# Kernel tuning notes

Measured on AMD Instinct MI355X. Metric: run time of the kernel, lower is better.

## Reference

```python
import jax, jax.numpy as jnp
import numpy as np

B, H, W, DIM, WS, SHIFT, HEADS = 32, 56, 56, 256, 7, 3, 8
N = WS * WS          # 49 tokens per window
C2 = 2 * DIM         # concatenated two-modal channel dim
NW = (H // WS) * (W // WS)


def _rel_index(ws):
    coords = np.stack(np.meshgrid(np.arange(ws), np.arange(ws), indexing='ij')).reshape(2, -1)
    rel = (coords[:, :, None] - coords[:, None, :]).transpose(1, 2, 0)
    rel[:, :, 0] += ws - 1
    rel[:, :, 1] += ws - 1
    rel[:, :, 0] *= 2 * ws - 1
    return rel.sum(-1)  # (N, N) int

REL_IDX = _rel_index(WS).reshape(-1)


def _attn_mask():
    # standard Swin shifted-window mask: 0 / -100 per window pair
    img = np.zeros((H, W))
    cnt = 0
    for hs in (slice(0, H - WS), slice(H - WS, H - SHIFT), slice(H - SHIFT, H)):
        for ws_ in (slice(0, W - WS), slice(W - WS, W - SHIFT), slice(W - SHIFT, W)):
            img[hs, ws_] = cnt
            cnt += 1
    mw = img.reshape(H // WS, WS, W // WS, WS).transpose(0, 2, 1, 3).reshape(-1, N)
    d = mw[:, None, :] - mw[:, :, None]
    return np.where(d != 0, -100.0, 0.0).astype(np.float32)  # (nW, N, N)

ATTN_MASK = _attn_mask()


def _win_part(x):  # (B,H,W,C) -> (nW*B, N, C)
    b, c = x.shape[0], x.shape[-1]
    x = x.reshape(b, H // WS, WS, W // WS, WS, c).transpose(0, 1, 3, 2, 4, 5)
    return x.reshape(-1, N, c)


def _win_rev(w, b):  # (nW*B, N, C) -> (B,H,W,C)
    c = w.shape[-1]
    x = w.reshape(b, H // WS, W // WS, WS, WS, c).transpose(0, 1, 3, 2, 4, 5)
    return x.reshape(b, H, W, c)


def _ln(t, g, bb):
    m = t.mean(-1, keepdims=True)
    v = t.var(-1, keepdims=True)
    return (t - m) / jnp.sqrt(v + 1e-5) * g + bb


def setup_inputs() -> dict:
    key = jax.random.key(0)
    ks = jax.random.split(key, 8)
    def nrm(k, shape, s=0.02):
        return jax.random.normal(k, shape, jnp.float32) * s
    return {
        'x': jax.random.normal(ks[0], (B, H * W, DIM), jnp.float32),
        'y': jax.random.normal(ks[1], (B, H * W, DIM), jnp.float32),
        'g1': jnp.ones((DIM,), jnp.float32), 'b1': jnp.zeros((DIM,), jnp.float32),
        'rpb': nrm(ks[2], ((2 * WS - 1) * (2 * WS - 1), HEADS)),
        'w_qkv': nrm(ks[3], (6 * DIM, 2 * DIM)), 'b_qkv': jnp.zeros((6 * DIM,), jnp.float32),
        'w_proj': nrm(ks[4], (DIM, 2 * DIM)), 'b_proj': jnp.zeros((DIM,), jnp.float32),
        'g2': jnp.ones((DIM,), jnp.float32), 'b2': jnp.zeros((DIM,), jnp.float32),
        'w_fc1': nrm(ks[5], (4 * DIM, DIM)), 'b_fc1': jnp.zeros((4 * DIM,), jnp.float32),
        'w_fc2': nrm(ks[6], (DIM, 4 * DIM)), 'b_fc2': jnp.zeros((DIM,), jnp.float32),
    }


def reference(x, y, g1, b1, rpb, w_qkv, b_qkv, w_proj, b_proj, g2, b2, w_fc1, b_fc1, w_fc2, b_fc2):
    scale = (DIM // HEADS) ** -0.5  # as in __init__: head_dim = dim // num_heads
    shortcut = x
    xn = _ln(x, g1, b1).reshape(B, H, W, DIM)
    yn = _ln(y, g1, b1).reshape(B, H, W, DIM)
    # cyclic shift
    xn = jnp.roll(xn, (-SHIFT, -SHIFT), axis=(1, 2))
    yn = jnp.roll(yn, (-SHIFT, -SHIFT), axis=(1, 2))
    xw, yw = _win_part(xn), _win_part(yn)            # (nW*B, N, C)
    xy = jnp.concatenate([xw, yw], axis=-1)          # (nW*B, N, 2C)
    nwb, hd = xy.shape[0], C2 // HEADS
    qkv = (xy @ w_qkv.T + b_qkv).reshape(nwb, N, 3, HEADS, hd).transpose(2, 0, 3, 1, 4)
    q, k, v = qkv[0] * scale, qkv[1], qkv[2]         # (nW*B, h, N, d)
    attn = jnp.einsum('whnd,whmd->whnm', q, k)
    bias = rpb[REL_IDX].reshape(N, N, HEADS).transpose(2, 0, 1)  # (h, N, N)
    attn = attn + bias[None]
    attn = attn.reshape(B, NW, HEADS, N, N) + jnp.asarray(ATTN_MASK)[None, :, None]
    attn = jax.nn.softmax(attn.reshape(nwb, HEADS, N, N), axis=-1)
    out = jnp.einsum('whnm,whmd->whnd', attn, v).transpose(0, 2, 1, 3).reshape(nwb, N, C2)
    out = out @ w_proj.T + b_proj                    # fuse 2C -> C
    out = _win_rev(out, B)
    out = jnp.roll(out, (SHIFT, SHIFT), axis=(1, 2)).reshape(B, H * W, DIM)
    x = shortcut + out
    h = _ln(x, g2, b2)
    h = jax.nn.gelu(h @ w_fc1.T + b_fc1, approximate=False)
    return x + h @ w_fc2.T + b_fc2
```

## Files before the change

### kernel.cpp

```cpp
#include <hip/hip_runtime.h>
#include <hip/hip_bf16.h>

#define DEVI __device__ __forceinline__

typedef __attribute__((ext_vector_type(8))) short short8;
typedef __attribute__((ext_vector_type(4))) float f32x4;
typedef unsigned int u32;
typedef unsigned short u16;

typedef __attribute__((address_space(1))) const u32 gu32_t;
typedef __attribute__((address_space(3))) u32 lu32_t;

DEVI u16 f2bf(float f) {
  u32 u = __builtin_bit_cast(u32, f);
  u32 r = (u + 0x7fffu + ((u >> 16) & 1u)) >> 16;
  return (u16)r;
}

DEVI f32x4 mfma16(short8 a, short8 b, f32x4 c) {
  return __builtin_amdgcn_mfma_f32_16x16x32_bf16(a, b, c, 0, 0, 0);
}

DEVI void gload16(const void* g, void* l) {
  __builtin_amdgcn_global_load_lds((gu32_t*)g, (lu32_t*)l, 16, 0, 0);
}

DEVI float gelu_t(float v) {
  const float u = v * (0.7978845608f + 0.0356774081f * v * v);
  const float t = 1.0f - 2.0f / (__expf(2.0f * u) + 1.0f);
  return 0.5f * v * (1.0f + t);
}

#define CHUNK_ROWS 25088
#define PLANE ((size_t)CHUNK_ROWS * 64)
#define KOFF  ((size_t)8 * PLANE)
#define VOFF  ((size_t)16 * PLANE)

__global__ __launch_bounds__(256) void convk(const float* __restrict__ s, u16* __restrict__ d, int n4) {
  int i = blockIdx.x * 256 + threadIdx.x;
  if (i < n4) {
    const float4 v = ((const float4*)s)[i];
    ushort4 o;
    o.x = f2bf(v.x); o.y = f2bf(v.y); o.z = f2bf(v.z); o.w = f2bf(v.w);
    ((ushort4*)d)[i] = o;
  }
}

__global__ __launch_bounds__(256) void btab_build(const float* __restrict__ rpb, float* __restrict__ btab) {
  const int cls = blockIdx.x >> 3, h = blockIdx.x & 7;
  float* dst = btab + (size_t)(cls * 8 + h) * 4096;
  for (int e = threadIdx.x; e < 4096; e += 256) {
    const int n = e >> 6, m = e & 63;
    float v;
    if (m >= 49) {
      v = -1e30f;
    } else if (n >= 49) {
      v = 0.f;
    } else {
      const int r1 = n / 7, c1 = n - r1 * 7;
      const int r2 = m / 7, c2 = m - r2 * 7;
      const int rel = (r1 - r2 + 6) * 13 + (c1 - c2 + 6);
      v = rpb[rel * 8 + h];
      const int reg1 = ((cls & 1) ? (r1 < 4 ? 1 : 2) : 0) * 3 + ((cls & 2) ? (c1 < 4 ? 1 : 2) : 0);
      const int reg2 = ((cls & 1) ? (r2 < 4 ? 1 : 2) : 0) * 3 + ((cls & 2) ? (c2 < 4 ? 1 : 2) : 0);
      if (reg1 != reg2) v -= 100.f;
    }
    dst[e] = v;
  }
}

__global__ __launch_bounds__(256) void ln_gather(
    const float* __restrict__ x, const float* __restrict__ y,
    const float* __restrict__ g1, const float* __restrict__ b1,
    u16* __restrict__ XY, int rowbase)
{
  const int wv = threadIdx.x >> 6, lane = threadIdx.x & 63;
  const int rl = blockIdx.x * 4 + wv;
  const int row = rowbase + rl;
  const int w = row / 49, n = row - w * 49;
  const int b = w >> 6, win = w & 63, wh = win >> 3, ww = win & 7;
  const int r = n / 7, c = n - r * 7;
  int oh = wh * 7 + r + 3; if (oh >= 56) oh -= 56;
  int ow = ww * 7 + c + 3; if (ow >= 56) ow -= 56;
  const size_t po = ((size_t)b * 3136 + oh * 56 + ow) * 256;
  const float4 g1v = ((const float4*)g1)[lane];
  const float4 b1v = ((const float4*)b1)[lane];
  u16* orow = XY + (size_t)rl * 512;
  #pragma unroll
  for (int mod = 0; mod < 2; ++mod) {
    const float* src = (mod ? y : x) + po;
    const float4 v = ((const float4*)src)[lane];
    float s = v.x + v.y + v.z + v.w;
    #pragma unroll
    for (int off = 1; off < 64; off <<= 1) s += __shfl_xor(s, off);
    const float mean = s * (1.0f / 256.0f);
    const float d0 = v.x - mean, d1 = v.y - mean, d2 = v.z - mean, d3 = v.w - mean;
    float sq = d0 * d0 + d1 * d1 + d2 * d2 + d3 * d3;
    #pragma unroll
    for (int off = 1; off < 64; off <<= 1) sq += __shfl_xor(sq, off);
    const float rstd = rsqrtf(sq * (1.0f / 256.0f) + 1e-5f);
    ushort4 o;
    o.x = f2bf(d0 * rstd * g1v.x + b1v.x);
    o.y = f2bf(d1 * rstd * g1v.y + b1v.y);
    o.z = f2bf(d2 * rstd * g1v.z + b1v.z);
    o.w = f2bf(d3 * rstd * g1v.w + b1v.w);
    *(ushort4*)(orow + mod * 256 + lane * 4) = o;
  }
}

__global__ __launch_bounds__(256) void qkv_gemm(
    const u16* __restrict__ A, const u16* __restrict__ Bw,
    const float* __restrict__ bias, u16* __restrict__ Qo)
{
  __shared__ __align__(16) u16 sA[128 * 64];
  __shared__ __align__(16) u16 sB[128 * 64];
  const int nx = gridDim.x;
  const int nwg = nx * gridDim.y;
  const int orig = blockIdx.y * nx + blockIdx.x;
  const int sw = (orig & 7) * (nwg >> 3) + (orig >> 3);
  const int m0  = (sw / nx) * 128;
  const int nn0 = (sw % nx) * 128;
  const int tid = threadIdx.x;
  const int lane = tid & 63;
  const int wv = tid >> 6;
  const int wm = wv >> 1, wn = wv & 1;
  const int rq = lane & 15, kg = lane >> 4;
  f32x4 acc[4][4];
  #pragma unroll
  for (int i = 0; i < 4; ++i)
    #pragma unroll
    for (int j = 0; j < 4; ++j) acc[i][j] = f32x4{0,0,0,0};

  for (int kt = 0; kt < 8; ++kt) {
    if (kt) __syncthreads();
    #pragma unroll
    for (int i = 0; i < 4; ++i) {
      const int c = i * 256 + tid;
      gload16(A + (size_t)(m0 + (c >> 3)) * 512 + kt * 64 + (c & 7) * 8, sA + c * 8);
    }
    #pragma unroll
    for (int i = 0; i < 4; ++i) {
      const int c = i * 256 + tid;
      gload16(Bw + (size_t)(nn0 + (c >> 3)) * 512 + kt * 64 + (c & 7) * 8, sB + c * 8);
    }
    __syncthreads();
    #pragma unroll
    for (int k0 = 0; k0 < 2; ++k0) {
      short8 af[4], bf8[4];
      #pragma unroll
      for (int mt = 0; mt < 4; ++mt)
        af[mt] = *(const short8*)(sA + (wm * 64 + mt * 16 + rq) * 64 + k0 * 32 + kg * 8);
      #pragma unroll
      for (int nt = 0; nt < 4; ++nt)
        bf8[nt] = *(const short8*)(sB + (wn * 64 + nt * 16 + rq) * 64 + k0 * 32 + kg * 8);
      #pragma unroll
      for (int mt = 0; mt < 4; ++mt)
        #pragma unroll
        for (int nt = 0; nt < 4; ++nt)
          acc[mt][nt] = mfma16(af[mt], bf8[nt], acc[mt][nt]);
    }
  }
  #pragma unroll
  for (int mt = 0; mt < 4; ++mt) {
    #pragma unroll
    for (int nt = 0; nt < 4; ++nt) {
      const int col = nn0 + wn * 64 + nt * 16 + rq;
      const int t = col >> 9, rem = col & 511;
      const int h = rem >> 6, d = rem & 63;
      const float bc = bias[col];
      const float sc = (t == 0) ? 0.17677669529663687f : 1.0f;
      u16* bp = Qo + (size_t)(t * 8 + h) * PLANE + d;
      #pragma unroll
      for (int r = 0; r < 4; ++r) {
        const int row = m0 + wm * 64 + mt * 16 + kg * 4 + r;
        bp[(size_t)row * 64] = f2bf((acc[mt][nt][r] + bc) * sc);
      }
    }
  }
}

__global__ __launch_bounds__(256, 3) void attn3(
    const u16* __restrict__ qkv, const float* __restrict__ btab,
    u16* __restrict__ concat, int wbase)
{
  __shared__ __align__(16) u16 sP[4][3136];
  __shared__ __align__(16) u16 sVT[4][4608];

  const int tid = threadIdx.x;
  const int wv = tid >> 6, lane = tid & 63;
  const int rq = lane & 15, kg = lane >> 4;
  const int gw = blockIdx.x * 4 + wv;
  const int wl = gw >> 3, h = gw & 7;
  const int w = wbase + wl;
  const int win = w & 63, wh = win >> 3, ww = win & 7;
  const int cls = ((wh == 7) ? 1 : 0) | ((ww == 7) ? 2 : 0);
  const float* Tb = btab + (size_t)(cls * 8 + h) * 4096;
  u16* sPw = sP[wv];
  u16* sVw = sVT[wv];

  const u16* qbase = qkv + (size_t)h * PLANE + (size_t)wl * 49 * 64;
  const u16* kbase = qkv + KOFF + (size_t)h * PLANE + (size_t)wl * 49 * 64;
  const u16* vbase = qkv + VOFF + (size_t)h * PLANE + (size_t)wl * 49 * 64;

  short8 vreg[4][2];
  #pragma unroll
  for (int t = 0; t < 4; ++t)
    #pragma unroll
    for (int h2 = 0; h2 < 2; ++h2)
      vreg[t][h2] = *(const short8*)(vbase + (size_t)(16 * t + rq) * 64 + kg * 8 + h2 * 32);

  short8 ak[4][2];
  #pragma unroll
  for (int j = 0; j < 4; ++j) {
    const int rr = (16 * j + rq) > 48 ? 48 : (16 * j + rq);
    ak[j][0] = *(const short8*)(kbase + rr * 64 + kg * 8);
    ak[j][1] = *(const short8*)(kbase + rr * 64 + 32 + kg * 8);
  }
  f32x4 sacc[4][4];
  #pragma unroll
  for (int i = 0; i < 4; ++i)
    #pragma unroll
    for (int j = 0; j < 4; ++j) sacc[i][j] = f32x4{0,0,0,0};
  #pragma unroll
  for (int i = 0; i < 4; ++i) {
    const int rr = (16 * i + rq) > 48 ? 48 : (16 * i + rq);
    const short8 a0 = *(const short8*)(qbase + rr * 64 + kg * 8);
    const short8 a1 = *(const short8*)(qbase + rr * 64 + 32 + kg * 8);
    #pragma unroll
    for (int j = 0; j < 4; ++j) {
      sacc[i][j] = mfma16(a0, ak[j][0], sacc[i][j]);
      sacc[i][j] = mfma16(a1, ak[j][1], sacc[i][j]);
    }
  }

  #pragma unroll
  for (int t = 0; t < 4; ++t) {
    const int row = 16 * t + rq;
    #pragma unroll
    for (int h2 = 0; h2 < 2; ++h2) {
      const int c0 = kg * 8 + h2 * 32;
      #pragma unroll
      for (int j = 0; j < 8; ++j)
        sVw[(c0 + j) * 72 + (row ^ (kg << 4))] = (u16)vreg[t][h2][j];
    }
  }

  #pragma unroll
  for (int i = 0; i < 4; ++i) {
    #pragma unroll
    for (int r = 0; r < 4; ++r) {
      const int n = 16 * i + kg * 4 + r;
      const float* Trow = Tb + n * 64 + rq;
      float pv[4];
      #pragma unroll
      for (int j = 0; j < 4; ++j)
        pv[j] = sacc[i][j][r] + Trow[16 * j];
      float mx = fmaxf(fmaxf(pv[0], pv[1]), fmaxf(pv[2], pv[3]));
      #pragma unroll
      for (int off = 1; off < 16; off <<= 1) mx = fmaxf(mx, __shfl_xor(mx, off));
      float sm = 0.f;
      #pragma unroll
      for (int j = 0; j < 4; ++j) { const float e = __expf(pv[j] - mx); pv[j] = e; sm += e; }
      #pragma unroll
      for (int off = 1; off < 16; off <<= 1) sm += __shfl_xor(sm, off);
      const float inv = 1.0f / sm;
      if (n < 49) {
        #pragma unroll
        for (int j = 0; j < 4; ++j) {
          const int col = 16 * j + rq;
          sPw[n * 64 + (((col >> 3) ^ (n & 7)) << 3) + (col & 7)] = f2bf(pv[j] * inv);
        }
      }
    }
  }

  f32x4 oacc[4][4];
  #pragma unroll
  for (int i = 0; i < 4; ++i)
    #pragma unroll
    for (int j = 0; j < 4; ++j) oacc[i][j] = f32x4{0,0,0,0};
  #pragma unroll
  for (int m0v = 0; m0v < 2; ++m0v) {
    short8 av[4];
    #pragma unroll
    for (int ct = 0; ct < 4; ++ct) {
      const int col = ct * 16 + rq;
      const int s = (col >> 3) & 3;
      short8 vvv = *(const short8*)(sVw + col * 72 + ((m0v * 32 + kg * 8) ^ (s << 4)));
      if (m0v == 1) {
        if (kg == 3) {
          #pragma unroll
          for (int e = 0; e < 8; ++e) vvv[e] = 0;
        } else if (kg == 2) {
          #pragma unroll
          for (int e = 1; e < 8; ++e) vvv[e] = 0;
        }
      }
      av[ct] = vvv;
    }
    #pragma unroll
    for (int i = 0; i < 4; ++i) {
      const int rr = (16 * i + rq) > 48 ? 48 : (16 * i + rq);
      const int ch = (m0v * 4 + kg) ^ (rr & 7);
      const short8 pa = *(const short8*)(sPw + rr * 64 + ch * 8);
      #pragma unroll
      for (int ct = 0; ct < 4; ++ct)
        oacc[i][ct] = mfma16(pa, av[ct], oacc[i][ct]);
    }
  }

  __builtin_amdgcn_s_waitcnt(0);
  #pragma unroll
  for (int i = 0; i < 4; ++i)
    #pragma unroll
    for (int ct = 0; ct < 4; ++ct)
      #pragma unroll
      for (int r = 0; r < 4; ++r) {
        const int n = 16 * i + kg * 4 + r;
        if (n < 49) {
          const int col = ct * 16 + rq;
          sPw[n * 64 + (((col >> 3) ^ (n & 7)) << 3) + (col & 7)] = f2bf(oacc[i][ct][r]);
        }
      }
  u16* crow = concat + (size_t)(wl * 49) * 512 + h * 64;
  #pragma unroll
  for (int it = 0; it < 7; ++it) {
    const int c = it * 64 + lane;
    if (c < 392) {
      const int m = c >> 3, s = c & 7;
      const short8 vvv = *(const short8*)(sPw + m * 64 + ((s ^ (m & 7)) << 3));
      *(short8*)(crow + (size_t)m * 512 + s * 8) = vvv;
    }
  }
}

__global__ __launch_bounds__(256, 2) void projln(
    const u16* __restrict__ A, const u16* __restrict__ Bw,
    const float* __restrict__ bias, const float* __restrict__ x,
    const float* __restrict__ g2, const float* __restrict__ b2,
    float* __restrict__ out, u16* __restrict__ xn2, int rowbase)
{
  __shared__ __align__(16) u16 sA[128 * 64];
  __shared__ __align__(16) u16 sB[256 * 64];
  const int m0 = blockIdx.x * 128;
  const int tid = threadIdx.x;
  const int lane = tid & 63;
  const int wv = tid >> 6;
  const int rq = lane & 15, kg = lane >> 4;
  f32x4 acc[2][16];
  #pragma unroll
  for (int i = 0; i < 2; ++i)
    #pragma unroll
    for (int j = 0; j < 16; ++j) acc[i][j] = f32x4{0,0,0,0};

  for (int kt = 0; kt < 8; ++kt) {
    if (kt) __syncthreads();
    #pragma unroll
    for (int i = 0; i < 4; ++i) {
      const int c = i * 256 + tid;
      gload16(A + (size_t)(m0 + (c >> 3)) * 512 + kt * 64 + (c & 7) * 8, sA + c * 8);
    }
    #pragma unroll
    for (int i = 0; i < 8; ++i) {
      const int c = i * 256 + tid;
      gload16(Bw + (size_t)(c >> 3) * 512 + kt * 64 + (c & 7) * 8, sB + c * 8);
    }
    __syncthreads();
    #pragma unroll
    for (int k0 = 0; k0 < 2; ++k0) {
      short8 af[2];
      #pragma unroll
      for (int mt = 0; mt < 2; ++mt)
        af[mt] = *(const short8*)(sA + (wv * 32 + mt * 16 + rq) * 64 + k0 * 32 + kg * 8);
      #pragma unroll
      for (int nt = 0; nt < 16; ++nt) {
        const short8 bf8 = *(const short8*)(sB + (nt * 16 + rq) * 64 + k0 * 32 + kg * 8);
        #pragma unroll
        for (int mt = 0; mt < 2; ++mt)
          acc[mt][nt] = mfma16(af[mt], bf8, acc[mt][nt]);
      }
    }
  }

  float br[16], g2r[16], b2r[16];
  #pragma unroll
  for (int nt = 0; nt < 16; ++nt) {
    const int col = nt * 16 + rq;
    br[nt] = bias[col]; g2r[nt] = g2[col]; b2r[nt] = b2[col];
  }
  #pragma unroll
  for (int mt = 0; mt < 2; ++mt) {
    #pragma unroll
    for (int r = 0; r < 4; ++r) {
      const int row = m0 + wv * 32 + mt * 16 + kg * 4 + r;
      const u32 g = (u32)(rowbase + row);
      const u32 w = g / 49u; const u32 n = g - w * 49u;
      const int b = w >> 6, win = w & 63, wh = win >> 3, ww = win & 7;
      const u32 rr = n / 7u; const u32 cc = n - rr * 7u;
      int oh = wh * 7 + (int)rr + 3; if (oh >= 56) oh -= 56;
      int ow = ww * 7 + (int)cc + 3; if (ow >= 56) ow -= 56;
      const size_t po = ((size_t)b * 3136 + oh * 56 + ow) * 256;
      float vals[16];
      float s = 0.f;
      #pragma unroll
      for (int nt = 0; nt < 16; ++nt) {
        const float v = acc[mt][nt][r] + br[nt] + x[po + nt * 16 + rq];
        vals[nt] = v; s += v;
      }
      #pragma unroll
      for (int off = 1; off < 16; off <<= 1) s += __shfl_xor(s, off);
      const float mean = s * (1.0f / 256.0f);
      float sq = 0.f;
      #pragma unroll
      for (int nt = 0; nt < 16; ++nt) { const float d_ = vals[nt] - mean; sq += d_ * d_; }
      #pragma unroll
      for (int off = 1; off < 16; off <<= 1) sq += __shfl_xor(sq, off);
      const float rstd = rsqrtf(sq * (1.0f / 256.0f) + 1e-5f);
      #pragma unroll
      for (int nt = 0; nt < 16; ++nt) {
        const int col = nt * 16 + rq;
        out[po + col] = vals[nt];
        xn2[po + col] = f2bf((vals[nt] - mean) * rstd * g2r[nt] + b2r[nt]);
      }
    }
  }
}

__global__ __launch_bounds__(256, 3) void fused_mlp(
    const u16* __restrict__ xn2, const u16* __restrict__ w1,
    const float* __restrict__ bf1, const u16* __restrict__ w2,
    const float* __restrict__ bf2v, float* __restrict__ out)
{
  __shared__ __align__(16) u16 sX[64 * 256];
  __shared__ __align__(16) u16 sH[64 * 128];

  const int m0 = blockIdx.x * 64;
  const int tid = threadIdx.x;
  const int wv = tid >> 6, lane = tid & 63;
  const int rq = lane & 15, kg = lane >> 4;

  #pragma unroll
  for (int i = 0; i < 8; ++i) {
    const int c = i * 256 + tid;
    const int row = c >> 5, ch = c & 31;
    const int sch = (ch & 24) | ((ch ^ row) & 7);
    gload16(xn2 + (size_t)(m0 + row) * 256 + sch * 8, sX + c * 8);
  }

  f32x4 acc2[4][4];
  #pragma unroll
  for (int i = 0; i < 4; ++i)
    #pragma unroll
    for (int j = 0; j < 4; ++j) acc2[i][j] = f32x4{0,0,0,0};

  __syncthreads();

  for (int t = 0; t < 8; ++t) {
    f32x4 a1[4][2];
    #pragma unroll
    for (int i = 0; i < 4; ++i)
      #pragma unroll
      for (int j = 0; j < 2; ++j) a1[i][j] = f32x4{0,0,0,0};
    #pragma unroll
    for (int ks = 0; ks < 8; ++ks) {
      short8 bfr[2];
      #pragma unroll
      for (int nt = 0; nt < 2; ++nt)
        bfr[nt] = *(const short8*)(w1 + (size_t)(t * 128 + wv * 32 + nt * 16 + rq) * 256 + ks * 32 + kg * 8);
      #pragma unroll
      for (int mt = 0; mt < 4; ++mt) {
        const int R = mt * 16 + rq;
        const int wk = ks * 4 + kg;
        const short8 af = *(const short8*)(sX + R * 256 + ((wk & 24) | ((wk ^ R) & 7)) * 8);
        #pragma unroll
        for (int nt = 0; nt < 2; ++nt)
          a1[mt][nt] = mfma16(af, bfr[nt], a1[mt][nt]);
      }
    }
    __syncthreads();
    #pragma unroll
    for (int nt = 0; nt < 2; ++nt) {
      const int col = wv * 32 + nt * 16 + rq;
      const float bb = bf1[t * 128 + col];
      const int ch = col >> 3;
      #pragma unroll
      for (int mt = 0; mt < 4; ++mt)
        #pragma unroll
        for (int r = 0; r < 4; ++r) {
          const int row = mt * 16 + kg * 4 + r;
          sH[row * 128 + ((ch & 8) | ((ch ^ row) & 7)) * 8 + (col & 7)] =
              f2bf(gelu_t(a1[mt][nt][r] + bb));
        }
    }
    __syncthreads();
    #pragma unroll
    for (int ks = 0; ks < 4; ++ks) {
      short8 bfr2[4];
      #pragma unroll
      for (int nt = 0; nt < 4; ++nt)
        bfr2[nt] = *(const short8*)(w2 + (size_t)(wv * 64 + nt * 16 + rq) * 1024 + t * 128 + ks * 32 + kg * 8);
      #pragma unroll
      for (int mt = 0; mt < 4; ++mt) {
        const int R = mt * 16 + rq;
        const int wk = ks * 4 + kg;
        const short8 af = *(const short8*)(sH + R * 128 + ((wk & 8) | ((wk ^ R) & 7)) * 8);
        #pragma unroll
        for (int nt = 0; nt < 4; ++nt)
          acc2[mt][nt] = mfma16(af, bfr2[nt], acc2[mt][nt]);
      }
    }
  }

  #pragma unroll
  for (int nt = 0; nt < 4; ++nt) {
    const int col = wv * 64 + nt * 16 + rq;
    const float bb = bf2v[col];
    #pragma unroll
    for (int mt = 0; mt < 4; ++mt)
      #pragma unroll
      for (int r = 0; r < 4; ++r) {
        float* p = out + (size_t)(m0 + mt * 16 + kg * 4 + r) * 256 + col;
        *p = acc2[mt][nt][r] + bb + *p;
      }
  }
}

extern "C" void kernel_launch(void* const* d_in, const int* in_sizes, int n_in,
                              void* d_out, int out_size, void* d_ws, size_t ws_size,
                              hipStream_t stream) {
  const float* x      = (const float*)d_in[0];
  const float* y      = (const float*)d_in[1];
  const float* g1     = (const float*)d_in[2];
  const float* b1     = (const float*)d_in[3];
  const float* rpb    = (const float*)d_in[4];
  const float* w_qkv  = (const float*)d_in[5];
  const float* b_qkv  = (const float*)d_in[6];
  const float* w_proj = (const float*)d_in[7];
  const float* b_proj = (const float*)d_in[8];
  const float* g2     = (const float*)d_in[9];
  const float* b2     = (const float*)d_in[10];
  const float* w_fc1  = (const float*)d_in[11];
  const float* b_fc1  = (const float*)d_in[12];
  const float* w_fc2  = (const float*)d_in[13];
  const float* b_fc2  = (const float*)d_in[14];
  float* out = (float*)d_out;

  u16* wsp = (u16*)d_ws;
  u16* wqkv_bf  = wsp;
  u16* wproj_bf = wsp + 786432;
  u16* wfc1_bf  = wsp + 917504;
  u16* wfc2_bf  = wsp + 1179648;
  float* btab   = (float*)(wsp + 1441792);
  u16* xn2      = wsp + 1703936;
  u16* XYc      = wsp + 27394048;
  u16* qkvc     = wsp + 40239104;

  convk<<<768, 256, 0, stream>>>(w_qkv,  wqkv_bf,  196608);
  convk<<<128, 256, 0, stream>>>(w_proj, wproj_bf, 32768);
  convk<<<256, 256, 0, stream>>>(w_fc1,  wfc1_bf,  65536);
  convk<<<256, 256, 0, stream>>>(w_fc2,  wfc2_bf,  65536);
  btab_build<<<32, 256, 0, stream>>>(rpb, btab);

  for (int c = 0; c < 4; ++c) {
    ln_gather<<<6272, 256, 0, stream>>>(x, y, g1, b1, XYc, c * CHUNK_ROWS);
    qkv_gemm<<<dim3(12, 196), 256, 0, stream>>>(XYc, wqkv_bf, b_qkv, qkvc);
    attn3<<<1024, 256, 0, stream>>>(qkvc, btab, XYc, c * 512);
    projln<<<196, 256, 0, stream>>>(XYc, wproj_bf, b_proj, x, g2, b2, out, xn2, c * CHUNK_ROWS);
  }

  fused_mlp<<<1568, 256, 0, stream>>>(xn2, wfc1_bf, b_fc1, wfc2_bf, b_fc2, out);
}
```

Measured before the change: 866.2 us.

## Stage QKV epilogue through LDS for coalesced stores; widen MLP hidden chunk

The QKV GEMM epilogue now writes bias-added, scaled bf16 results into a swizzled shared-memory tile that reuses the operand buffers. It then issues 16-byte vector stores per head plane, replacing the previous scattered 2-byte stores with a 128-byte row stride. Separately, the fused MLP processes the 1024-wide hidden dimension in 4 chunks of 256 instead of 8 of 128. This halves the barrier/GELU round trips but doubles sH and the accumulator registers, and lowers the occupancy hint from 3 to 2 blocks per CU.

Result: no change. 854.1 us (-1.4%).

```diff
diff --git a/kernel.cpp b/kernel.cpp
--- a/kernel.cpp
+++ b/kernel.cpp
@@ -112,8 +112,9 @@
     const u16* __restrict__ A, const u16* __restrict__ Bw,
     const float* __restrict__ bias, u16* __restrict__ Qo)
 {
-  __shared__ __align__(16) u16 sA[128 * 64];
-  __shared__ __align__(16) u16 sB[128 * 64];
+  __shared__ __align__(16) u16 smem[128 * 128];
+  u16* sA = smem;
+  u16* sB = smem + 128 * 64;
   const int nx = gridDim.x;
   const int nwg = nx * gridDim.y;
   const int orig = blockIdx.y * nx + blockIdx.x;
@@ -160,22 +161,33 @@
           acc[mt][nt] = mfma16(af[mt], bf8[nt], acc[mt][nt]);
     }
   }
-  #pragma unroll
-  for (int mt = 0; mt < 4; ++mt) {
-    #pragma unroll
-    for (int nt = 0; nt < 4; ++nt) {
-      const int col = nn0 + wn * 64 + nt * 16 + rq;
-      const int t = col >> 9, rem = col & 511;
-      const int h = rem >> 6, d = rem & 63;
-      const float bc = bias[col];
-      const float sc = (t == 0) ? 0.17677669529663687f : 1.0f;
-      u16* bp = Qo + (size_t)(t * 8 + h) * PLANE + d;
+  __syncthreads();
+  const int t = nn0 >> 9;
+  const int hbase = (nn0 & 511) >> 6;
+  const float sc = (t == 0) ? 0.17677669529663687f : 1.0f;
+  #pragma unroll
+  for (int nt = 0; nt < 4; ++nt) {
+    const int col = wn * 64 + nt * 16 + rq;
+    const float bc = bias[nn0 + col];
+    const int c = col >> 3;
+    #pragma unroll
+    for (int mt = 0; mt < 4; ++mt)
       #pragma unroll
       for (int r = 0; r < 4; ++r) {
-        const int row = m0 + wm * 64 + mt * 16 + kg * 4 + r;
-        bp[(size_t)row * 64] = f2bf((acc[mt][nt][r] + bc) * sc);
-      }
-    }
+        const int row = wm * 64 + mt * 16 + kg * 4 + r;
+        smem[row * 128 + (((c & 8) | ((c ^ row) & 7)) << 3) + (col & 7)] =
+            f2bf((acc[mt][nt][r] + bc) * sc);
+      }
+  }
+  __syncthreads();
+  #pragma unroll
+  for (int it = 0; it < 8; ++it) {
+    const int cc = it * 256 + tid;
+    const int row = cc >> 4, c = cc & 15;
+    const int col = c * 8;
+    const int hh = col >> 6, d = col & 63;
+    const short8 v = *(const short8*)(smem + row * 128 + (((c & 8) | ((c ^ row) & 7)) << 3));
+    *(short8*)(Qo + (size_t)(t * 8 + hbase + hh) * PLANE + (size_t)(m0 + row) * 64 + d) = v;
   }
 }
 
@@ -426,13 +438,13 @@
   }
 }
 
-__global__ __launch_bounds__(256, 3) void fused_mlp(
+__global__ __launch_bounds__(256, 2) void fused_mlp(
     const u16* __restrict__ xn2, const u16* __restrict__ w1,
     const float* __restrict__ bf1, const u16* __restrict__ w2,
     const float* __restrict__ bf2v, float* __restrict__ out)
 {
   __shared__ __align__(16) u16 sX[64 * 256];
-  __shared__ __align__(16) u16 sH[64 * 128];
+  __shared__ __align__(16) u16 sH[64 * 256];
 
   const int m0 = blockIdx.x * 64;
   const int tid = threadIdx.x;
@@ -455,55 +467,55 @@
 
   __syncthreads();
 
-  for (int t = 0; t < 8; ++t) {
-    f32x4 a1[4][2];
+  for (int t = 0; t < 4; ++t) {
+    f32x4 a1[4][4];
     #pragma unroll
     for (int i = 0; i < 4; ++i)
       #pragma unroll
-      for (int j = 0; j < 2; ++j) a1[i][j] = f32x4{0,0,0,0};
+      for (int j = 0; j < 4; ++j) a1[i][j] = f32x4{0,0,0,0};
     #pragma unroll
     for (int ks = 0; ks < 8; ++ks) {
-      short8 bfr[2];
-      #pragma unroll
-      for (int nt = 0; nt < 2; ++nt)
-        bfr[nt] = *(const short8*)(w1 + (size_t)(t * 128 + wv * 32 + nt * 16 + rq) * 256 + ks * 32 + kg * 8);
+      short8 bfr[4];
+      #pragma unroll
+      for (int nt = 0; nt < 4; ++nt)
+        bfr[nt] = *(const short8*)(w1 + (size_t)(t * 256 + wv * 64 + nt * 16 + rq) * 256 + ks * 32 + kg * 8);
       #pragma unroll
       for (int mt = 0; mt < 4; ++mt) {
         const int R = mt * 16 + rq;
         const int wk = ks * 4 + kg;
         const short8 af = *(const short8*)(sX + R * 256 + ((wk & 24) | ((wk ^ R) & 7)) * 8);
         #pragma unroll
-        for (int nt = 0; nt < 2; ++nt)
+        for (int nt = 0; nt < 4; ++nt)
           a1[mt][nt] = mfma16(af, bfr[nt], a1[mt][nt]);
       }
     }
     __syncthreads();
     #pragma unroll
-    for (int nt = 0; nt < 2; ++nt) {
-      const int col = wv * 32 + nt * 16 + rq;
-      const float bb = bf1[t * 128 + col];
-      const int ch = col >> 3;
+    for (int nt = 0; nt < 4; ++nt) {
+      const int col = wv * 64 + nt * 16 + rq;
+      const float bb = bf1[t * 256 + col];
+      const int c = col >> 3;
       #pragma unroll
       for (int mt = 0; mt < 4; ++mt)
         #pragma unroll
         for (int r = 0; r < 4; ++r) {
           const int row = mt * 16 + kg * 4 + r;
-          sH[row * 128 + ((ch & 8) | ((ch ^ row) & 7)) * 8 + (col & 7)] =
+          sH[row * 256 + ((c & 24) | ((c ^ row) & 7)) * 8 + (col & 7)] =
               f2bf(gelu_t(a1[mt][nt][r] + bb));
         }
     }
     __syncthreads();
     #pragma unroll
-    for (int ks = 0; ks < 4; ++ks) {
+    for (int ks = 0; ks < 8; ++ks) {
       short8 bfr2[4];
       #pragma unroll
       for (int nt = 0; nt < 4; ++nt)
-        bfr2[nt] = *(const short8*)(w2 + (size_t)(wv * 64 + nt * 16 + rq) * 1024 + t * 128 + ks * 32 + kg * 8);
+        bfr2[nt] = *(const short8*)(w2 + (size_t)(wv * 64 + nt * 16 + rq) * 1024 + t * 256 + ks * 32 + kg * 8);
       #pragma unroll
       for (int mt = 0; mt < 4; ++mt) {
         const int R = mt * 16 + rq;
         const int wk = ks * 4 + kg;
-        const short8 af = *(const short8*)(sH + R * 128 + ((wk & 8) | ((wk ^ R) & 7)) * 8);
+        const short8 af = *(const short8*)(sH + R * 256 + ((wk & 24) | ((wk ^ R) & 7)) * 8);
         #pragma unroll
         for (int nt = 0; nt < 4; ++nt)
           acc2[mt][nt] = mfma16(af, bfr2[nt], acc2[mt][nt]);
```
